# Performance work log

Measured on AMD Instinct MI355X. Metric: run time of the kernel, lower is better.

Reference implementation:

```python
import jax, jax.numpy as jnp
import numpy as np

B, N, K, C = 4, 8192, 16, 64
HID, OUT = 128, 128


def setup_inputs() -> dict:
    key = jax.random.key(0)
    ks = jax.random.split(key, 8)
    f = jax.random.normal(ks[0], (B, N, C), dtype=jnp.float32)
    knn_idx = jax.random.randint(ks[1], (B, N, K), 0, N, dtype=jnp.int32)
    W1 = jax.random.normal(ks[2], (3 * C, HID), dtype=jnp.float32) * (1.0 / np.sqrt(3 * C))
    b1 = jnp.zeros((HID,), dtype=jnp.float32)
    W2 = jax.random.normal(ks[3], (HID, HID), dtype=jnp.float32) * (1.0 / np.sqrt(HID))
    b2 = jnp.zeros((HID,), dtype=jnp.float32)
    W3 = jax.random.normal(ks[4], (HID, OUT), dtype=jnp.float32) * 0.05  # init.normal_(std=0.05)
    b3 = jnp.zeros((OUT,), dtype=jnp.float32)  # init.zeros_
    return {"f": f, "knn_idx": knn_idx, "W1": W1, "b1": b1, "W2": W2, "b2": b2, "W3": W3, "b3": b3}


def reference(f, knn_idx, W1, b1, W2, b2, W3, b3):
    # knn_group: gather neighbor features -> [B, N, k, C]
    knn_feat = jax.vmap(lambda fb, ib: fb[ib])(f, knn_idx)
    f_tiled = jnp.broadcast_to(f[:, :, None, :], knn_feat.shape)  # [B,N,k,C]
    x = jnp.concatenate([f_tiled, knn_feat, knn_feat - f_tiled], axis=-1)  # [B,N,k,3C]
    x = jax.nn.relu(jnp.einsum('bnkc,ch->bnkh', x, W1) + b1)
    x = jax.nn.relu(jnp.einsum('bnkh,hg->bnkg', x, W2) + b2)
    x = jnp.max(x, axis=2)  # max-pool over k -> [B,N,HID]
    return jnp.einsum('bnh,ho->bno', x, W3) + b3
```

## Files before the change

kernel.cpp:

```cpp
#include <hip/hip_runtime.h>


#define BB 4
#define NN 8192
#define KK 16
#define CC 64
#define HH 128

typedef _Float16 f16;
typedef _Float16 f16x8 __attribute__((ext_vector_type(8)));
typedef float f32x4 __attribute__((ext_vector_type(4)));

#define MFMA16(a, b, c) __builtin_amdgcn_mfma_f32_16x16x32_f16(a, b, c, 0, 0, 0)

__global__ void prep_pack(const float* __restrict__ W1, const float* __restrict__ W2,
                          const float* __restrict__ W3, f16* __restrict__ ws) {
  int fid = blockIdx.x;
  int l = threadIdx.x;
  int g = l >> 4, r = l & 15;
  f16x8 v;
#pragma unroll
  for (int j = 0; j < 8; ++j) {
    int kl = 16 * (j >> 2) + 4 * g + (j & 3);
    float x;
    if (fid < 32) {
      int ht = fid >> 2, kt = fid & 3, h = ht * 16 + r;
      if (kt < 2) {
        int k = kt * 32 + kl;
        x = W1[(64 + k) * HH + h] + W1[(128 + k) * HH + h];
      } else {
        int k = (kt - 2) * 32 + kl;
        x = W1[k * HH + h] - W1[(128 + k) * HH + h];
      }
    } else if (fid < 64) {
      int t = fid - 32, h2t = t >> 2, kt = t & 3;
      x = W2[(kt * 32 + kl) * HH + h2t * 16 + r];
    } else {
      int t = fid - 64, ot = t >> 2, kt = t & 3;
      x = W3[(kt * 32 + kl) * HH + ot * 16 + r];
    }
    v[j] = (f16)x;
  }
  *(f16x8*)(ws + (size_t)fid * 512 + l * 8) = v;
}

__global__ __launch_bounds__(512, 4) void knn_main(
    const float* __restrict__ f, const int* __restrict__ knn,
    const float* __restrict__ b1, const float* __restrict__ b2,
    const float* __restrict__ b3, const f16* __restrict__ ws,
    float* __restrict__ out) {
  extern __shared__ char smem[];
  f16* wbuf = (f16*)smem;
  f16* pooled = wbuf + 64 * 512;

  const int tid = threadIdx.x;
  const int wave = tid >> 6, lane = tid & 63;
  const int g = lane >> 4, r = lane & 15;

  const int wg = (blockIdx.x & 7) * 256 + (blockIdx.x >> 3);
  const int b = wg >> 9;
  const int n0 = (wg & 511) * 16;
  const float* fb = f + (size_t)b * NN * CC;
  const int p0 = wave * 2;

  int nidx[2];
#pragma unroll
  for (int pp = 0; pp < 2; ++pp)
    nidx[pp] = knn[(size_t)(b * NN + n0 + p0 + pp) * KK + r];

  f16x8 stmp[8];
#pragma unroll
  for (int i = 0; i < 8; ++i)
    stmp[i] = *(const f16x8*)(ws + (size_t)(i * 512 + tid) * 8);
#pragma unroll
  for (int i = 0; i < 8; ++i)
    *(f16x8*)(wbuf + (size_t)(i * 512 + tid) * 8) = stmp[i];

  f16x8 bf[2][4];
#pragma unroll
  for (int pp = 0; pp < 2; ++pp) {
    const float* frow = fb + (size_t)nidx[pp] * CC;
    const float* fown = fb + (size_t)(n0 + p0 + pp) * CC;
#pragma unroll
    for (int kt = 0; kt < 4; ++kt) {
      const float* src = (kt < 2) ? (frow + kt * 32) : (fown + (kt - 2) * 32);
      f32x4 a0 = *(const f32x4*)(src + 4 * g);
      f32x4 a1 = *(const f32x4*)(src + 4 * g + 16);
#pragma unroll
      for (int jl = 0; jl < 4; ++jl) {
        bf[pp][kt][jl] = (f16)a0[jl];
        bf[pp][kt][4 + jl] = (f16)a1[jl];
      }
    }
  }

  __syncthreads();

  f16x8 h1f[2][4];
#pragma unroll
  for (int ht = 0; ht < 8; ++ht) {
    f32x4 acc[2] = {{0.f, 0.f, 0.f, 0.f}, {0.f, 0.f, 0.f, 0.f}};
#pragma unroll
    for (int kt = 0; kt < 4; ++kt) {
      f16x8 wfrag = *(const f16x8*)(wbuf + (size_t)(ht * 4 + kt) * 512 + lane * 8);
      acc[0] = MFMA16(wfrag, bf[0][kt], acc[0]);
      acc[1] = MFMA16(wfrag, bf[1][kt], acc[1]);
    }
    f32x4 b1v = *(const f32x4*)(b1 + ht * 16 + g * 4);
#pragma unroll
    for (int pp = 0; pp < 2; ++pp)
#pragma unroll
      for (int i = 0; i < 4; ++i) {
        float x = acc[pp][i] + b1v[i];
        h1f[pp][ht >> 1][(ht & 1) * 4 + i] = (f16)(x > 0.f ? x : 0.f);
      }
  }

#pragma unroll
  for (int h2t = 0; h2t < 8; ++h2t) {
    f32x4 acc[2] = {{0.f, 0.f, 0.f, 0.f}, {0.f, 0.f, 0.f, 0.f}};
#pragma unroll
    for (int kt = 0; kt < 4; ++kt) {
      f16x8 w2f = *(const f16x8*)(wbuf + (size_t)(32 + h2t * 4 + kt) * 512 + lane * 8);
      acc[0] = MFMA16(h1f[0][kt], w2f, acc[0]);
      acc[1] = MFMA16(h1f[1][kt], w2f, acc[1]);
    }
    float b2v = b2[h2t * 16 + r];
#pragma unroll
    for (int pp = 0; pp < 2; ++pp) {
      float m = fmaxf(fmaxf(acc[pp][0], acc[pp][1]), fmaxf(acc[pp][2], acc[pp][3]));
      m = fmaxf(m, __shfl_xor(m, 16, 64));
      m = fmaxf(m, __shfl_xor(m, 32, 64));
      float x = m + b2v;
      f16 pv = (f16)(x > 0.f ? x : 0.f);
      if (g == 0) {
        pooled[(h2t >> 1) * 512 + ((r >> 2) * 16 + (p0 + pp)) * 8 +
               (h2t & 1) * 4 + (r & 3)] = pv;
      }
    }
  }

  __syncthreads();

  {
    f32x4 acc3 = {0.f, 0.f, 0.f, 0.f};
#pragma unroll
    for (int kt = 0; kt < 4; ++kt) {
      f16x8 w3f = *(const f16x8*)(ws + (size_t)(64 + wave * 4 + kt) * 512 + lane * 8);
      f16x8 pf = *(const f16x8*)(pooled + kt * 512 + lane * 8);
      acc3 = MFMA16(w3f, pf, acc3);
    }
    f32x4 b3v = *(const f32x4*)(b3 + wave * 16 + g * 4);
    f32x4 o;
#pragma unroll
    for (int i = 0; i < 4; ++i) o[i] = acc3[i] + b3v[i];
    *(f32x4*)(out + ((size_t)b * NN + n0 + r) * HH + wave * 16 + g * 4) = o;
  }
}

extern "C" void kernel_launch(void* const* d_in, const int* in_sizes, int n_in,
                              void* d_out, int out_size, void* d_ws, size_t ws_size,
                              hipStream_t stream) {
  const float* f = (const float*)d_in[0];
  const int* knn = (const int*)d_in[1];
  const float* W1 = (const float*)d_in[2];
  const float* b1 = (const float*)d_in[3];
  const float* W2 = (const float*)d_in[4];
  const float* b2 = (const float*)d_in[5];
  const float* W3 = (const float*)d_in[6];
  const float* b3 = (const float*)d_in[7];
  float* outp = (float*)d_out;
  f16* wsp = (f16*)d_ws;

  (void)hipFuncSetAttribute((const void*)knn_main,
                            hipFuncAttributeMaxDynamicSharedMemorySize, 69632);

  prep_pack<<<96, 64, 0, stream>>>(W1, W2, W3, wsp);
  knn_main<<<(BB * NN) / 16, 512, 69632, stream>>>(f, knn, b1, b2, b3, wsp, outp);
}
```

Baseline: 55.31 us.

## Hoist per-point W1 term out of neighbor loop and process four tiles per block

```diff
diff --git a/kernel.cpp b/kernel.cpp
--- a/kernel.cpp
+++ b/kernel.cpp
@@ -6,6 +6,7 @@
 #define KK 16
 #define CC 64
 #define HH 128
+#define ITERS 4
 
 typedef _Float16 f16;
 typedef _Float16 f16x8 __attribute__((ext_vector_type(8)));
@@ -23,18 +24,15 @@
   for (int j = 0; j < 8; ++j) {
     int kl = 16 * (j >> 2) + 4 * g + (j & 3);
     float x;
-    if (fid < 32) {
-      int ht = fid >> 2, kt = fid & 3, h = ht * 16 + r;
-      if (kt < 2) {
-        int k = kt * 32 + kl;
-        x = W1[(64 + k) * HH + h] + W1[(128 + k) * HH + h];
-      } else {
-        int k = (kt - 2) * 32 + kl;
-        x = W1[k * HH + h] - W1[(128 + k) * HH + h];
-      }
+    if (fid < 16) {
+      int ht = fid >> 1, kt = fid & 1, h = ht * 16 + r, k = kt * 32 + kl;
+      x = W1[(64 + k) * HH + h] + W1[(128 + k) * HH + h];
+    } else if (fid < 48) {
+      int t = fid - 16, h2t = t >> 2, kt = t & 3;
+      x = W2[(kt * 32 + kl) * HH + h2t * 16 + r];
     } else if (fid < 64) {
-      int t = fid - 32, h2t = t >> 2, kt = t & 3;
-      x = W2[(kt * 32 + kl) * HH + h2t * 16 + r];
+      int t = fid - 48, ht = t >> 1, kt = t & 1, h = ht * 16 + r, k = kt * 32 + kl;
+      x = W1[k * HH + h] - W1[(128 + k) * HH + h];
     } else {
       int t = fid - 64, ot = t >> 2, kt = t & 3;
       x = W3[(kt * 32 + kl) * HH + ot * 16 + r];
@@ -51,110 +49,157 @@
     float* __restrict__ out) {
   extern __shared__ char smem[];
   f16* wbuf = (f16*)smem;
-  f16* pooled = wbuf + 64 * 512;
+  float* fabuf = (float*)(wbuf + 48 * 512);
+  f16* pooled = (f16*)(fabuf + 2 * 16 * 132);
 
   const int tid = threadIdx.x;
   const int wave = tid >> 6, lane = tid & 63;
   const int g = lane >> 4, r = lane & 15;
 
-  const int wg = (blockIdx.x & 7) * 256 + (blockIdx.x >> 3);
-  const int b = wg >> 9;
-  const int n0 = (wg & 511) * 16;
+  const int wg = (blockIdx.x & 7) * 64 + (blockIdx.x >> 3);
+  const int b = wg >> 7;
+  const int nbase = (wg & 127) * 64;
   const float* fb = f + (size_t)b * NN * CC;
   const int p0 = wave * 2;
 
+  f16x8 st[6];
+#pragma unroll
+  for (int i = 0; i < 6; ++i)
+    st[i] = *(const f16x8*)(ws + (size_t)(i * 512 + tid) * 8);
+#pragma unroll
+  for (int i = 0; i < 6; ++i)
+    *(f16x8*)(wbuf + (size_t)(i * 512 + tid) * 8) = st[i];
+
   int nidx[2];
 #pragma unroll
   for (int pp = 0; pp < 2; ++pp)
-    nidx[pp] = knn[(size_t)(b * NN + n0 + p0 + pp) * KK + r];
-
-  f16x8 stmp[8];
-#pragma unroll
-  for (int i = 0; i < 8; ++i)
-    stmp[i] = *(const f16x8*)(ws + (size_t)(i * 512 + tid) * 8);
-#pragma unroll
-  for (int i = 0; i < 8; ++i)
-    *(f16x8*)(wbuf + (size_t)(i * 512 + tid) * 8) = stmp[i];
-
-  f16x8 bf[2][4];
-#pragma unroll
-  for (int pp = 0; pp < 2; ++pp) {
-    const float* frow = fb + (size_t)nidx[pp] * CC;
-    const float* fown = fb + (size_t)(n0 + p0 + pp) * CC;
-#pragma unroll
-    for (int kt = 0; kt < 4; ++kt) {
-      const float* src = (kt < 2) ? (frow + kt * 32) : (fown + (kt - 2) * 32);
-      f32x4 a0 = *(const f32x4*)(src + 4 * g);
-      f32x4 a1 = *(const f32x4*)(src + 4 * g + 16);
-#pragma unroll
-      for (int jl = 0; jl < 4; ++jl) {
-        bf[pp][kt][jl] = (f16)a0[jl];
-        bf[pp][kt][4 + jl] = (f16)a1[jl];
-      }
-    }
-  }
-
-  __syncthreads();
-
-  f16x8 h1f[2][4];
-#pragma unroll
-  for (int ht = 0; ht < 8; ++ht) {
-    f32x4 acc[2] = {{0.f, 0.f, 0.f, 0.f}, {0.f, 0.f, 0.f, 0.f}};
-#pragma unroll
-    for (int kt = 0; kt < 4; ++kt) {
-      f16x8 wfrag = *(const f16x8*)(wbuf + (size_t)(ht * 4 + kt) * 512 + lane * 8);
-      acc[0] = MFMA16(wfrag, bf[0][kt], acc[0]);
-      acc[1] = MFMA16(wfrag, bf[1][kt], acc[1]);
-    }
-    f32x4 b1v = *(const f32x4*)(b1 + ht * 16 + g * 4);
+    nidx[pp] = knn[((size_t)b * NN + nbase + p0 + pp) * KK + r];
+
+  for (int it = 0; it < ITERS; ++it) {
+    const int n0 = nbase + it * 16;
+    const int buf = it & 1;
+
+    f32x4 rawA[2][2][2];
+#pragma unroll
+    for (int pp = 0; pp < 2; ++pp) {
+      const float* frow = fb + (size_t)nidx[pp] * CC;
+#pragma unroll
+      for (int kt = 0; kt < 2; ++kt) {
+        rawA[pp][kt][0] = *(const f32x4*)(frow + kt * 32 + 4 * g);
+        rawA[pp][kt][1] = *(const f32x4*)(frow + kt * 32 + 4 * g + 16);
+      }
+    }
+    const float* fo = fb + (size_t)(n0 + r) * CC;
+    f32x4 rawO[2][2];
+#pragma unroll
+    for (int kt = 0; kt < 2; ++kt) {
+      rawO[kt][0] = *(const f32x4*)(fo + kt * 32 + 4 * g);
+      rawO[kt][1] = *(const f32x4*)(fo + kt * 32 + 4 * g + 16);
+    }
+    const int itn = (it < ITERS - 1) ? it + 1 : it;
+    int nidn[2];
 #pragma unroll
     for (int pp = 0; pp < 2; ++pp)
+      nidn[pp] = knn[((size_t)b * NN + nbase + itn * 16 + p0 + pp) * KK + r];
+
+    {
+      f32x4 acc = {0.f, 0.f, 0.f, 0.f};
+#pragma unroll
+      for (int kt = 0; kt < 2; ++kt) {
+        f16x8 aw = *(const f16x8*)(ws + (size_t)(48 + wave * 2 + kt) * 512 + lane * 8);
+        f16x8 bfa;
+#pragma unroll
+        for (int jl = 0; jl < 4; ++jl) {
+          bfa[jl] = (f16)rawO[kt][0][jl];
+          bfa[4 + jl] = (f16)rawO[kt][1][jl];
+        }
+        acc = MFMA16(aw, bfa, acc);
+      }
+      f32x4 b1v = *(const f32x4*)(b1 + wave * 16 + g * 4);
+      f32x4 fa;
+#pragma unroll
+      for (int i = 0; i < 4; ++i) fa[i] = acc[i] + b1v[i];
+      *(f32x4*)(fabuf + buf * 2112 + r * 132 + wave * 16 + g * 4) = fa;
+    }
+
+    __syncthreads();
+
+    f16x8 bf[2][2];
+#pragma unroll
+    for (int pp = 0; pp < 2; ++pp)
+#pragma unroll
+      for (int kt = 0; kt < 2; ++kt)
+#pragma unroll
+        for (int jl = 0; jl < 4; ++jl) {
+          bf[pp][kt][jl] = (f16)rawA[pp][kt][0][jl];
+          bf[pp][kt][4 + jl] = (f16)rawA[pp][kt][1][jl];
+        }
+
+    f16x8 h1f[2][4];
+#pragma unroll
+    for (int ht = 0; ht < 8; ++ht) {
+      f16x8 w0 = *(const f16x8*)(wbuf + (size_t)(ht * 2 + 0) * 512 + lane * 8);
+      f16x8 w1 = *(const f16x8*)(wbuf + (size_t)(ht * 2 + 1) * 512 + lane * 8);
+      f32x4 a0 = {0.f, 0.f, 0.f, 0.f}, a1 = {0.f, 0.f, 0.f, 0.f};
+      a0 = MFMA16(w0, bf[0][0], a0);
+      a0 = MFMA16(w1, bf[0][1], a0);
+      a1 = MFMA16(w0, bf[1][0], a1);
+      a1 = MFMA16(w1, bf[1][1], a1);
+      f32x4 fa0 = *(const f32x4*)(fabuf + buf * 2112 + (p0 + 0) * 132 + ht * 16 + g * 4);
+      f32x4 fa1 = *(const f32x4*)(fabuf + buf * 2112 + (p0 + 1) * 132 + ht * 16 + g * 4);
 #pragma unroll
       for (int i = 0; i < 4; ++i) {
-        float x = acc[pp][i] + b1v[i];
-        h1f[pp][ht >> 1][(ht & 1) * 4 + i] = (f16)(x > 0.f ? x : 0.f);
-      }
-  }
-
-#pragma unroll
-  for (int h2t = 0; h2t < 8; ++h2t) {
-    f32x4 acc[2] = {{0.f, 0.f, 0.f, 0.f}, {0.f, 0.f, 0.f, 0.f}};
-#pragma unroll
-    for (int kt = 0; kt < 4; ++kt) {
-      f16x8 w2f = *(const f16x8*)(wbuf + (size_t)(32 + h2t * 4 + kt) * 512 + lane * 8);
-      acc[0] = MFMA16(h1f[0][kt], w2f, acc[0]);
-      acc[1] = MFMA16(h1f[1][kt], w2f, acc[1]);
-    }
-    float b2v = b2[h2t * 16 + r];
-#pragma unroll
-    for (int pp = 0; pp < 2; ++pp) {
-      float m = fmaxf(fmaxf(acc[pp][0], acc[pp][1]), fmaxf(acc[pp][2], acc[pp][3]));
-      m = fmaxf(m, __shfl_xor(m, 16, 64));
-      m = fmaxf(m, __shfl_xor(m, 32, 64));
-      float x = m + b2v;
-      f16 pv = (f16)(x > 0.f ? x : 0.f);
-      if (g == 0) {
-        pooled[(h2t >> 1) * 512 + ((r >> 2) * 16 + (p0 + pp)) * 8 +
-               (h2t & 1) * 4 + (r & 3)] = pv;
-      }
-    }
-  }
-
-  __syncthreads();
-
-  {
-    f32x4 acc3 = {0.f, 0.f, 0.f, 0.f};
-#pragma unroll
-    for (int kt = 0; kt < 4; ++kt) {
-      f16x8 w3f = *(const f16x8*)(ws + (size_t)(64 + wave * 4 + kt) * 512 + lane * 8);
-      f16x8 pf = *(const f16x8*)(pooled + kt * 512 + lane * 8);
-      acc3 = MFMA16(w3f, pf, acc3);
-    }
-    f32x4 b3v = *(const f32x4*)(b3 + wave * 16 + g * 4);
-    f32x4 o;
-#pragma unroll
-    for (int i = 0; i < 4; ++i) o[i] = acc3[i] + b3v[i];
-    *(f32x4*)(out + ((size_t)b * NN + n0 + r) * HH + wave * 16 + g * 4) = o;
+        float x0 = a0[i] + fa0[i];
+        float x1 = a1[i] + fa1[i];
+        h1f[0][ht >> 1][(ht & 1) * 4 + i] = (f16)(x0 > 0.f ? x0 : 0.f);
+        h1f[1][ht >> 1][(ht & 1) * 4 + i] = (f16)(x1 > 0.f ? x1 : 0.f);
+      }
+    }
+
+#pragma unroll
+    for (int h2t = 0; h2t < 8; ++h2t) {
+      f32x4 c0 = {0.f, 0.f, 0.f, 0.f}, c1 = {0.f, 0.f, 0.f, 0.f};
+#pragma unroll
+      for (int kt = 0; kt < 4; ++kt) {
+        f16x8 w2f = *(const f16x8*)(wbuf + (size_t)(16 + h2t * 4 + kt) * 512 + lane * 8);
+        c0 = MFMA16(h1f[0][kt], w2f, c0);
+        c1 = MFMA16(h1f[1][kt], w2f, c1);
+      }
+      float b2v = b2[h2t * 16 + r];
+#pragma unroll
+      for (int pp = 0; pp < 2; ++pp) {
+        f32x4 cc = pp ? c1 : c0;
+        float m = fmaxf(fmaxf(cc[0], cc[1]), fmaxf(cc[2], cc[3]));
+        m = fmaxf(m, __shfl_xor(m, 16, 64));
+        m = fmaxf(m, __shfl_xor(m, 32, 64));
+        float x = m + b2v;
+        f16 pv = (f16)(x > 0.f ? x : 0.f);
+        if (g == 0) {
+          pooled[buf * 2048 + (h2t >> 1) * 512 + ((r >> 2) * 16 + p0 + pp) * 8 +
+                 (h2t & 1) * 4 + (r & 3)] = pv;
+        }
+      }
+    }
+
+    __syncthreads();
+
+    {
+      f32x4 a3 = {0.f, 0.f, 0.f, 0.f};
+#pragma unroll
+      for (int kt = 0; kt < 4; ++kt) {
+        f16x8 w3f = *(const f16x8*)(ws + (size_t)(64 + wave * 4 + kt) * 512 + lane * 8);
+        f16x8 pf = *(const f16x8*)(pooled + buf * 2048 + kt * 512 + lane * 8);
+        a3 = MFMA16(w3f, pf, a3);
+      }
+      f32x4 b3v = *(const f32x4*)(b3 + wave * 16 + g * 4);
+      f32x4 o;
+#pragma unroll
+      for (int i = 0; i < 4; ++i) o[i] = a3[i] + b3v[i];
+      *(f32x4*)(out + ((size_t)b * NN + n0 + r) * HH + wave * 16 + g * 4) = o;
+    }
+
+    nidx[0] = nidn[0];
+    nidx[1] = nidn[1];
   }
 }
 
@@ -173,8 +218,8 @@
   f16* wsp = (f16*)d_ws;
 
   (void)hipFuncSetAttribute((const void*)knn_main,
-                            hipFuncAttributeMaxDynamicSharedMemorySize, 69632);
+                            hipFuncAttributeMaxDynamicSharedMemorySize, 74240);
 
   prep_pack<<<96, 64, 0, stream>>>(W1, W2, W3, wsp);
-  knn_main<<<(BB * NN) / 16, 512, 69632, stream>>>(f, knn, b1, b2, b3, wsp, outp);
+  knn_main<<<(BB * NN) / (16 * ITERS), 512, 74240, stream>>>(f, knn, b1, b2, b3, wsp, outp);
 }
```

New measurement: 68.43 us. 1.24x slower.
